# Performance work log

Measured on AMD Instinct MI355X. Metric: run time of the kernel, lower is better.

Reference implementation:

```python
import jax, jax.numpy as jnp
import numpy as np

N_NODES = 100000


def setup_inputs() -> dict:
    key = jax.random.key(0)
    ks = jax.random.split(key, 10)
    N, T, IN, H, OUT = N_NODES, 20, 1, 64, 1
    E = 3200000
    s = 1.0 / np.sqrt(H)
    return {
        "x": jax.random.normal(ks[0], (N, T, IN), dtype=jnp.float32),
        "edge_index": jax.random.randint(ks[1], (E, 2), 0, N, dtype=jnp.int64),
        "W_ih": jax.random.uniform(ks[2], (H, IN), jnp.float32, -s, s),
        "b_ih": jax.random.uniform(ks[3], (H,), jnp.float32, -s, s),
        "W_hh": jax.random.uniform(ks[4], (H, H), jnp.float32, -s, s),
        "b_hh": jax.random.uniform(ks[5], (H,), jnp.float32, -s, s),
        "W_gcn": jax.random.uniform(ks[6], (H, H), jnp.float32, -s, s),
        "b_gcn": jax.random.uniform(ks[7], (H,), jnp.float32, -s, s),
        "W_fc": jax.random.uniform(ks[8], (OUT, H), jnp.float32, -s, s),
        "b_fc": jax.random.uniform(ks[9], (OUT,), jnp.float32, -s, s),
    }


def _strnn_fwd(x, edge_index, W_ih, b_ih, W_hh, b_hh, W_gcn, b_gcn, W_fc, b_fc):
    N = x.shape[0]
    H = W_hh.shape[0]

    # ---- vanilla tanh RNN (batch_first); only last hidden state is needed ----
    xs = jnp.swapaxes(x, 0, 1)  # [T, N, in]

    def step(h, xt):
        h = jnp.tanh(xt @ W_ih.T + b_ih + h @ W_hh.T + b_hh)
        return h, None

    h_last, _ = jax.lax.scan(step, jnp.zeros((N, H), x.dtype), xs)  # [N, H]

    # ---- GCNConv: add self-loops, sym-normalize, linear, scatter-add ----
    src = edge_index[:, 0]
    dst = edge_index[:, 1]
    loop = jnp.arange(N, dtype=src.dtype)
    src = jnp.concatenate([src, loop])
    dst = jnp.concatenate([dst, loop])

    xw = h_last @ W_gcn.T  # [N, H]
    deg = jax.ops.segment_sum(jnp.ones_like(dst, dtype=xw.dtype), dst, num_segments=N)
    dinv = jnp.where(deg > 0, jax.lax.rsqrt(deg), 0.0)
    norm = dinv[src] * dinv[dst]  # [E+N]

    msgs = xw[src] * norm[:, None]  # gather + scale, [E+N, H]
    agg = jax.ops.segment_sum(msgs, dst, num_segments=N) + b_gcn  # scatter-add

    return agg @ W_fc.T + b_fc  # [N, out]


def reference(x, edge_index, W_ih, b_ih, W_hh, b_hh, W_gcn, b_gcn, W_fc, b_fc):
    return _strnn_fwd(x, edge_index, W_ih, b_ih, W_hh, b_hh, W_gcn, b_gcn, W_fc, b_fc)
```

## Files before the change

kernel.cpp:

```cpp
#include <hip/hip_runtime.h>

#define TT 20
#define HH 64
#define RSZ 16384
#define DRSZ 32768
#define NSL 64

typedef __attribute__((ext_vector_type(8))) short short8;
typedef __attribute__((ext_vector_type(4))) float f32x4;

__device__ __forceinline__ unsigned fbits(float f) { union { float f; unsigned u; } v; v.f = f; return v.u; }
__device__ __forceinline__ float bcast(unsigned u) { union { float f; unsigned u; } v; v.u = u; return v.f; }

__global__ __launch_bounds__(1024) void k_deg_bin(const int* __restrict__ ei,
                                                  unsigned* __restrict__ degrep,
                                                  int N, int E, int R, int N2) {
    __shared__ unsigned bin[DRSZ / 2];
    const int r = blockIdx.x % R;
    const int s = blockIdx.x / R;
    const int base = r * DRSZ;
    for (int i = threadIdx.x; i < DRSZ / 2; i += 1024) bin[i] = 0;
    __syncthreads();
    const long long eb = (long long)s * E / NSL;
    const long long ee = (long long)(s + 1) * E / NSL;
    const int2* ei2 = (const int2*)ei;
    for (long long e = eb + threadIdx.x; e < ee; e += 1024) {
        int2 p = ei2[e];
        unsigned u = (unsigned)(p.y - base);
        if (u < DRSZ) atomicAdd(&bin[u >> 1], 1u << ((u & 1) << 4));
    }
    __syncthreads();
    const int lim = min(DRSZ, N - base);
    const int words = (lim + 1) >> 1;
    unsigned* dst = degrep + (size_t)s * N2 + (base >> 1);
    for (int i = threadIdx.x; i < words; i += 1024) dst[i] = bin[i];
}

__global__ __launch_bounds__(256, 3) void k_rnn(
    const float* __restrict__ x,
    const float* __restrict__ W_ih, const float* __restrict__ b_ih,
    const float* __restrict__ W_hh, const float* __restrict__ b_hh,
    const float* __restrict__ W_gcn, const float* __restrict__ W_fc,
    float* __restrict__ z, int N)
{
    __shared__ __align__(16) unsigned short sHh[4][1024];
    __shared__ __align__(16) unsigned short sHl[4][1024];
    __shared__ __align__(16) float sX[4][16 * TT];

    const int t    = threadIdx.x;
    const int w    = t >> 6;
    const int l    = t & 63;
    const int nl   = l & 15;
    const int quad = l >> 4;
    const int n0   = blockIdx.x * 64 + w * 16;

    unsigned short* hh = sHh[w];
    unsigned short* hl = sHl[w];
    float*          sx = sX[w];

    for (int i = l; i < 16 * TT; i += 64) {
        int nn = i / TT, tt = i - nn * TT;
        int n = n0 + nn; if (n >= N) n = N - 1;
        sx[tt * 16 + nn] = x[(size_t)n * TT + tt];
    }
    {
        uint4 zz = {0, 0, 0, 0};
        uint4* ph = (uint4*)hh;
        uint4* pl = (uint4*)hl;
#pragma unroll
        for (int i = 0; i < 2; ++i) { ph[l + 64 * i] = zz; pl[l + 64 * i] = zz; }
    }

    short8 Bh[4][2], Bl[4][2];
#pragma unroll
    for (int tt2 = 0; tt2 < 4; ++tt2)
#pragma unroll
        for (int kc = 0; kc < 2; ++kc) {
            const float* wr = W_hh + (size_t)(16 * tt2 + nl) * HH + kc * 32 + quad * 8;
            float4 w0 = *(const float4*)(wr);
            float4 w1 = *(const float4*)(wr + 4);
            float wvv[8] = {w0.x, w0.y, w0.z, w0.w, w1.x, w1.y, w1.z, w1.w};
            short8 sh, sl;
#pragma unroll
            for (int j = 0; j < 8; ++j) {
                unsigned u  = fbits(wvv[j]);
                unsigned hb = u & 0xffff0000u;
                float lo = wvv[j] - bcast(hb);
                sh[j] = (short)(hb >> 16);
                sl[j] = (short)(fbits(lo) >> 16);
            }
            Bh[tt2][kc] = sh; Bl[tt2][kc] = sl;
        }

    float vl = 0.0f;
#pragma unroll 8
    for (int j = 0; j < HH; ++j) vl = fmaf(W_fc[j], W_gcn[j * HH + l], vl);

    float wih4[4], bs4[4], vv[4];
#pragma unroll
    for (int tt2 = 0; tt2 < 4; ++tt2) {
        int n = nl + 16 * tt2;
        wih4[tt2] = W_ih[n];
        bs4[tt2]  = b_ih[n] + b_hh[n];
        vv[tt2]   = __shfl(vl, n, 64);
    }

    const int ra = (l ^ ((l >> 4) & 1)) * 8;

    f32x4 C[4];

    for (int step = 0; step < TT; ++step) {
        const float4 xr = *(const float4*)&sx[step * 16 + quad * 4];
#pragma unroll
        for (int tt2 = 0; tt2 < 4; ++tt2) {
            C[tt2][0] = fmaf(xr.x, wih4[tt2], bs4[tt2]);
            C[tt2][1] = fmaf(xr.y, wih4[tt2], bs4[tt2]);
            C[tt2][2] = fmaf(xr.z, wih4[tt2], bs4[tt2]);
            C[tt2][3] = fmaf(xr.w, wih4[tt2], bs4[tt2]);
        }

#pragma unroll
        for (int kc = 0; kc < 2; ++kc) {
            short8 Ah = *(const short8*)&hh[kc * 512 + ra];
            short8 Al = *(const short8*)&hl[kc * 512 + ra];
#pragma unroll
            for (int tt2 = 0; tt2 < 4; ++tt2) {
                C[tt2] = __builtin_amdgcn_mfma_f32_16x16x32_bf16(Ah, Bh[tt2][kc], C[tt2], 0, 0, 0);
                C[tt2] = __builtin_amdgcn_mfma_f32_16x16x32_bf16(Ah, Bl[tt2][kc], C[tt2], 0, 0, 0);
                C[tt2] = __builtin_amdgcn_mfma_f32_16x16x32_bf16(Al, Bh[tt2][kc], C[tt2], 0, 0, 0);
            }
        }

#pragma unroll
        for (int tt2 = 0; tt2 < 4; ++tt2) {
            const int kc_d = tt2 >> 1;
            const int qa   = (nl >> 3) + 2 * (tt2 & 1);
            const int jj   = nl & 7;
#pragma unroll
            for (int r = 0; r < 4; ++r) {
                float eg = __builtin_amdgcn_exp2f(C[tt2][r] * 2.885390081777927f);
                float hv = fmaf(-2.0f, __builtin_amdgcn_rcpf(eg + 1.0f), 1.0f);
                C[tt2][r] = hv;
                unsigned um = fbits(hv);
                unsigned hb = um & 0xffff0000u;
                float lo = hv - bcast(hb);
                const int m   = quad * 4 + r;
                const int la  = m + 16 * qa;
                const int idx = kc_d * 512 + (la ^ ((la >> 4) & 1)) * 8 + jj;
                hh[idx] = (unsigned short)(um >> 16);
                hl[idx] = (unsigned short)(fbits(lo) >> 16);
            }
        }
    }

#pragma unroll
    for (int r = 0; r < 4; ++r) {
        float p = 0.0f;
#pragma unroll
        for (int tt2 = 0; tt2 < 4; ++tt2) p = fmaf(C[tt2][r], vv[tt2], p);
        p += __shfl_xor(p, 1, 64);
        p += __shfl_xor(p, 2, 64);
        p += __shfl_xor(p, 4, 64);
        p += __shfl_xor(p, 8, 64);
        if (nl == 0) {
            const int n = n0 + quad * 4 + r;
            if (n < N) z[n] = p;
        }
    }
}

__global__ __launch_bounds__(256) void k_w(const unsigned* __restrict__ degrep,
                                           const float* __restrict__ z,
                                           float* __restrict__ dinv,
                                           float* __restrict__ w, int N, int N2) {
    int n = blockIdx.x * blockDim.x + threadIdx.x;
    if (n >= N) return;
    const int wd = n >> 1, sh = (n & 1) << 4;
    unsigned d = 0;
#pragma unroll 8
    for (int s = 0; s < NSL; ++s) d += (degrep[(size_t)s * N2 + wd] >> sh) & 0xffffu;
    float di = __frsqrt_rn((float)d + 1.0f);
    dinv[n] = di;
    w[n] = di * z[n];
}

__global__ __launch_bounds__(1024) void k_edge_bin(const int* __restrict__ ei,
                                                   const float* __restrict__ w,
                                                   float* __restrict__ Srep,
                                                   int N, int E, int R) {
    __shared__ float bin[RSZ];
    const int r = blockIdx.x % R;
    const int s = blockIdx.x / R;
    const int base = r * RSZ;
    for (int i = threadIdx.x; i < RSZ; i += 1024) bin[i] = 0.0f;
    __syncthreads();
    const long long eb = (long long)s * E / NSL;
    const long long ee = (long long)(s + 1) * E / NSL;
    const int2* ei2 = (const int2*)ei;
    for (long long e = eb + threadIdx.x; e < ee; e += 1024) {
        int2 p = ei2[e];
        unsigned u = (unsigned)(p.y - base);
        if (u < RSZ) atomicAdd(&bin[u], w[p.x]);
    }
    __syncthreads();
    const int lim = min(RSZ, N - base);
    float* dst = Srep + (size_t)s * N + base;
    for (int i = threadIdx.x; i < lim; i += 1024) dst[i] = bin[i];
}

__global__ __launch_bounds__(256) void k_final(const float* __restrict__ dinv,
                                               const float* __restrict__ Srep,
                                               const float* __restrict__ w,
                                               const float* __restrict__ b_gcn,
                                               const float* __restrict__ W_fc,
                                               const float* __restrict__ b_fc,
                                               float* __restrict__ out, int N)
{
    float c = b_fc[0];
#pragma unroll 8
    for (int j = 0; j < HH; ++j) c = fmaf(W_fc[j], b_gcn[j], c);
    int n = blockIdx.x * blockDim.x + threadIdx.x;
    if (n >= N) return;
    float S = 0.0f;
#pragma unroll 8
    for (int s = 0; s < NSL; ++s) S += Srep[(size_t)s * N + n];
    float d = dinv[n];
    out[n] = fmaf(d, S, fmaf(d, w[n], c));
}

extern "C" void kernel_launch(void* const* d_in, const int* in_sizes, int n_in,
                              void* d_out, int out_size, void* d_ws, size_t ws_size,
                              hipStream_t stream)
{
    const float* x     = (const float*)d_in[0];
    const int*   ei    = (const int*)d_in[1];
    const float* W_ih  = (const float*)d_in[2];
    const float* b_ih  = (const float*)d_in[3];
    const float* W_hh  = (const float*)d_in[4];
    const float* b_hh  = (const float*)d_in[5];
    const float* W_gcn = (const float*)d_in[6];
    const float* b_gcn = (const float*)d_in[7];
    const float* W_fc  = (const float*)d_in[8];
    const float* b_fc  = (const float*)d_in[9];
    float* out = (float*)d_out;

    const int N  = in_sizes[0] / TT;
    const int E  = in_sizes[1] / 2;
    const int N2 = (N + 1) / 2;
    const int RD = (N + DRSZ - 1) / DRSZ;
    const int RS = (N + RSZ - 1) / RSZ;

    char* ws = (char*)d_ws;
    size_t off = 0;
    auto alloc = [&](size_t bytes) { void* p = ws + off; off += (bytes + 255) & ~(size_t)255; return p; };
    unsigned* degrep = (unsigned*)alloc((size_t)NSL * N2 * 4);
    float*    Srep   = (float*)   alloc((size_t)NSL * N * 4);
    float*    z      = (float*)   alloc((size_t)N * 4);
    float*    dinv   = (float*)   alloc((size_t)N * 4);
    float*    w      = (float*)   alloc((size_t)N * 4);

    const int rnnBlocks = (N + 63) / 64;
    k_deg_bin <<<RD * NSL, 1024, 0, stream>>>(ei, degrep, N, E, RD, N2);
    k_rnn     <<<rnnBlocks, 256, 0, stream>>>(x, W_ih, b_ih, W_hh, b_hh,
                                              W_gcn, W_fc, z, N);
    k_w       <<<(N + 255) / 256, 256, 0, stream>>>(degrep, z, dinv, w, N, N2);
    k_edge_bin<<<RS * NSL, 1024, 0, stream>>>(ei, w, Srep, N, E, RS);
    k_final   <<<(N + 255) / 256, 256, 0, stream>>>(dinv, Srep, w, b_gcn, W_fc, b_fc, out, N);
}
```

Measured before the change: 245.2 us.

## Fuse degree binning into RNN kernel and vectorize edge loads to int4

Merges the degree-histogram kernel into the RNN kernel as extra leading blocks, so degree counting and RNN compute share one launch and can run concurrently on the GPU. The degree bins are halved to 16K nodes with 32 edge slices and 256-thread blocks, so the two roles fit the same shared-memory footprint. Both the degree and edge-binning loops now load two edges per int4 read instead of one per int2, with a tail fix for odd E. The cost is more blocks per edge pass (more regions) and heterogeneous block roles sharing occupancy limits of the RNN's launch bounds.

```diff
diff --git a/kernel.cpp b/kernel.cpp
--- a/kernel.cpp
+++ b/kernel.cpp
@@ -3,8 +3,9 @@
 #define TT 20
 #define HH 64
 #define RSZ 16384
-#define DRSZ 32768
+#define DRSZ 16384
 #define NSL 64
+#define NSLD 32
 
 typedef __attribute__((ext_vector_type(8))) short short8;
 typedef __attribute__((ext_vector_type(4))) float f32x4;
@@ -12,51 +13,58 @@
 __device__ __forceinline__ unsigned fbits(float f) { union { float f; unsigned u; } v; v.f = f; return v.u; }
 __device__ __forceinline__ float bcast(unsigned u) { union { float f; unsigned u; } v; v.u = u; return v.f; }
 
-__global__ __launch_bounds__(1024) void k_deg_bin(const int* __restrict__ ei,
-                                                  unsigned* __restrict__ degrep,
-                                                  int N, int E, int R, int N2) {
-    __shared__ unsigned bin[DRSZ / 2];
-    const int r = blockIdx.x % R;
-    const int s = blockIdx.x / R;
-    const int base = r * DRSZ;
-    for (int i = threadIdx.x; i < DRSZ / 2; i += 1024) bin[i] = 0;
-    __syncthreads();
-    const long long eb = (long long)s * E / NSL;
-    const long long ee = (long long)(s + 1) * E / NSL;
-    const int2* ei2 = (const int2*)ei;
-    for (long long e = eb + threadIdx.x; e < ee; e += 1024) {
-        int2 p = ei2[e];
-        unsigned u = (unsigned)(p.y - base);
-        if (u < DRSZ) atomicAdd(&bin[u >> 1], 1u << ((u & 1) << 4));
-    }
-    __syncthreads();
-    const int lim = min(DRSZ, N - base);
-    const int words = (lim + 1) >> 1;
-    unsigned* dst = degrep + (size_t)s * N2 + (base >> 1);
-    for (int i = threadIdx.x; i < words; i += 1024) dst[i] = bin[i];
-}
-
-__global__ __launch_bounds__(256, 3) void k_rnn(
+__global__ __launch_bounds__(256, 3) void k_fused(
     const float* __restrict__ x,
     const float* __restrict__ W_ih, const float* __restrict__ b_ih,
     const float* __restrict__ W_hh, const float* __restrict__ b_hh,
     const float* __restrict__ W_gcn, const float* __restrict__ W_fc,
-    float* __restrict__ z, int N)
+    const int* __restrict__ ei, unsigned* __restrict__ degrep,
+    float* __restrict__ z, int N, int E, int RD, int N2)
 {
-    __shared__ __align__(16) unsigned short sHh[4][1024];
-    __shared__ __align__(16) unsigned short sHl[4][1024];
-    __shared__ __align__(16) float sX[4][16 * TT];
-
-    const int t    = threadIdx.x;
+    __shared__ __align__(16) unsigned smem[8192];
+
+    const int t = threadIdx.x;
+    const int RDN = RD * NSLD;
+
+    if (blockIdx.x < RDN) {
+        unsigned* bin = smem;
+        const int r = blockIdx.x % RD;
+        const int s = blockIdx.x / RD;
+        const int base = r * DRSZ;
+        for (int i = t; i < DRSZ / 2; i += 256) bin[i] = 0;
+        __syncthreads();
+        const long long P = (long long)(E >> 1);
+        const long long pb = s * P / NSLD;
+        const long long pe = (s + 1) * P / NSLD;
+        const int4* ei4 = (const int4*)ei;
+        for (long long g = pb + t; g < pe; g += 256) {
+            int4 q = ei4[g];
+            unsigned u0 = (unsigned)(q.y - base);
+            unsigned u1 = (unsigned)(q.w - base);
+            if (u0 < DRSZ) atomicAdd(&bin[u0 >> 1], 1u << ((u0 & 1) << 4));
+            if (u1 < DRSZ) atomicAdd(&bin[u1 >> 1], 1u << ((u1 & 1) << 4));
+        }
+        if ((E & 1) && s == NSLD - 1 && t == 0) {
+            unsigned u = (unsigned)(ei[2 * (E - 1) + 1] - base);
+            if (u < DRSZ) atomicAdd(&bin[u >> 1], 1u << ((u & 1) << 4));
+        }
+        __syncthreads();
+        const int lim = min(DRSZ, N - base);
+        const int words = (lim + 1) >> 1;
+        unsigned* dst = degrep + (size_t)s * N2 + (base >> 1);
+        for (int i = t; i < words; i += 256) dst[i] = bin[i];
+        return;
+    }
+
     const int w    = t >> 6;
     const int l    = t & 63;
     const int nl   = l & 15;
     const int quad = l >> 4;
-    const int n0   = blockIdx.x * 64 + w * 16;
-
-    unsigned short* hh = sHh[w];
-    unsigned short* hl = sHl[w];
-    float*          sx = sX[w];
+    const int n0   = (blockIdx.x - RDN) * 64 + w * 16;
+
+    unsigned short* hh = (unsigned short*)&smem[w * 512];
+    unsigned short* hl = (unsigned short*)&smem[2048 + w * 512];
+    float*          sx = (float*)&smem[4096 + w * 320];
 
     for (int i = l; i < 16 * TT; i += 64) {
         int nn = i / TT, tt = i - nn * TT;
@@ -178,7 +186,7 @@
     const int wd = n >> 1, sh = (n & 1) << 4;
     unsigned d = 0;
 #pragma unroll 8
-    for (int s = 0; s < NSL; ++s) d += (degrep[(size_t)s * N2 + wd] >> sh) & 0xffffu;
+    for (int s = 0; s < NSLD; ++s) d += (degrep[(size_t)s * N2 + wd] >> sh) & 0xffffu;
     float di = __frsqrt_rn((float)d + 1.0f);
     dinv[n] = di;
     w[n] = di * z[n];
@@ -194,13 +202,20 @@
     const int base = r * RSZ;
     for (int i = threadIdx.x; i < RSZ; i += 1024) bin[i] = 0.0f;
     __syncthreads();
-    const long long eb = (long long)s * E / NSL;
-    const long long ee = (long long)(s + 1) * E / NSL;
-    const int2* ei2 = (const int2*)ei;
-    for (long long e = eb + threadIdx.x; e < ee; e += 1024) {
-        int2 p = ei2[e];
-        unsigned u = (unsigned)(p.y - base);
-        if (u < RSZ) atomicAdd(&bin[u], w[p.x]);
+    const long long P = (long long)(E >> 1);
+    const long long pb = s * P / NSL;
+    const long long pe = (s + 1) * P / NSL;
+    const int4* ei4 = (const int4*)ei;
+    for (long long g = pb + threadIdx.x; g < pe; g += 1024) {
+        int4 q = ei4[g];
+        unsigned u0 = (unsigned)(q.y - base);
+        unsigned u1 = (unsigned)(q.w - base);
+        if (u0 < RSZ) atomicAdd(&bin[u0], w[q.x]);
+        if (u1 < RSZ) atomicAdd(&bin[u1], w[q.z]);
+    }
+    if ((E & 1) && s == NSL - 1 && threadIdx.x == 0) {
+        unsigned u = (unsigned)(ei[2 * (E - 1) + 1] - base);
+        if (u < RSZ) atomicAdd(&bin[u], w[ei[2 * (E - 1)]]);
     }
     __syncthreads();
     const int lim = min(RSZ, N - base);
@@ -253,16 +268,16 @@
     char* ws = (char*)d_ws;
     size_t off = 0;
     auto alloc = [&](size_t bytes) { void* p = ws + off; off += (bytes + 255) & ~(size_t)255; return p; };
-    unsigned* degrep = (unsigned*)alloc((size_t)NSL * N2 * 4);
+    unsigned* degrep = (unsigned*)alloc((size_t)NSLD * N2 * 4);
     float*    Srep   = (float*)   alloc((size_t)NSL * N * 4);
     float*    z      = (float*)   alloc((size_t)N * 4);
     float*    dinv   = (float*)   alloc((size_t)N * 4);
     float*    w      = (float*)   alloc((size_t)N * 4);
 
     const int rnnBlocks = (N + 63) / 64;
-    k_deg_bin <<<RD * NSL, 1024, 0, stream>>>(ei, degrep, N, E, RD, N2);
-    k_rnn     <<<rnnBlocks, 256, 0, stream>>>(x, W_ih, b_ih, W_hh, b_hh,
-                                              W_gcn, W_fc, z, N);
+    k_fused   <<<RD * NSLD + rnnBlocks, 256, 0, stream>>>(x, W_ih, b_ih, W_hh, b_hh,
+                                                          W_gcn, W_fc, ei, degrep,
+                                                          z, N, E, RD, N2);
     k_w       <<<(N + 255) / 256, 256, 0, stream>>>(degrep, z, dinv, w, N, N2);
     k_edge_bin<<<RS * NSL, 1024, 0, stream>>>(ei, w, Srep, N, E, RS);
     k_final   <<<(N + 255) / 256, 256, 0, stream>>>(dinv, Srep, w, b_gcn, W_fc, b_fc, out, N);
```

Measured after the change: 221.2 us. -9.8%, faster.
